# Performance work log

Measured on AMD Instinct MI355X. Metric: run time of the kernel, lower is better.

The kernel has to match this reference:

```python
import jax, jax.numpy as jnp
import numpy as np

N_GEN = 6
DIM = 1 << N_GEN  # 64
B, F = 256, 128
EPS = 1e-6


def _build_algebra():
    # Blades as bitmasks over N_GEN generators, canonical grade-then-lex order.
    blades = sorted(range(DIM), key=lambda b: (bin(b).count("1"), b))
    index = {b: i for i, b in enumerate(blades)}
    grades = np.array([bin(b).count("1") for b in blades], dtype=np.int64)
    cls = (grades % 4).astype(np.int32)  # quaternion-type class of each blade

    def swap_sign(a, b):
        s = 0
        a >>= 1
        while a:
            s += bin(a & b).count("1")
            a >>= 1
        return -1.0 if (s & 1) else 1.0

    # cayley[i, j, k] = coefficient of e_j in e_i * e_k (Euclidean metric, +1 squares)
    cayley = np.zeros((DIM, DIM, DIM), dtype=np.float32)
    for bi in range(DIM):
        for bk in range(DIM):
            cayley[index[bi], index[bi ^ bk], index[bk]] = swap_sign(bi, bk)

    # qt_geometric_product_paths: which (class_i, class_j, class_k) triples are nonzero
    paths = np.zeros((4, 4, 4), dtype=bool)
    i_, j_, k_ = np.nonzero(cayley)
    paths[cls[i_], cls[j_], cls[k_]] = True
    return cayley, cls, np.argwhere(paths).astype(np.int32)  # paths.sum() == 32


def setup_inputs() -> dict:
    cayley, cls, pidx = _build_algebra()
    P = pidx.shape[0]
    key = jax.random.key(0)
    k1, k2, k3 = jax.random.split(key, 3)
    x = jax.random.normal(k1, (B, F, DIM), jnp.float32)
    # reset_parameters: std = 1/sqrt(algebra.dim_generators + 1)
    w_gp = jax.random.normal(k2, (F, P), jnp.float32) / np.sqrt(N_GEN + 1)
    w_lin = jax.random.normal(k3, (F, F, 4), jnp.float32) / np.sqrt(F)
    b_lin = jnp.zeros((F,), jnp.float32)
    a_norm = jnp.zeros((F, 4), jnp.float32)  # normalization_init = 0
    return {"x": x, "w_gp": w_gp, "w_lin": w_lin, "b_lin": b_lin,
            "a_norm": a_norm, "cayley": jnp.asarray(cayley),
            "cls": jnp.asarray(cls), "path_idx": jnp.asarray(pidx)}


def reference(x, w_gp, w_lin, b_lin, a_norm, cayley, cls, path_idx):
    # --- QTLinear: per-QT-class channel mixing (weight shared within each class) ---
    w_lin_full = w_lin[:, :, cls]                          # [F_out, F_in, D]
    xr = jnp.einsum('bmi,nmi->bni', x, w_lin_full)         # [B, F, D]
    xr = xr.at[..., 0].add(b_lin)                          # bias on scalar blade only

    # --- QTNormalization: sigmoid-gated per-class norm, interpolated toward 1 ---
    sq = jnp.moveaxis(xr * xr, -1, 0)                      # [D, B, F]
    norms4 = jnp.sqrt(jax.ops.segment_sum(sq, cls, num_segments=4))  # [4, B, F]
    norms4 = jnp.moveaxis(norms4, 0, -1)                   # [B, F, 4]
    gated = jax.nn.sigmoid(a_norm) * (norms4 - 1.0) + 1.0  # [B, F, 4]
    xr = xr / (gated[..., cls] + EPS)                      # broadcast class norm to blades

    # --- _get_weight: scatter path weights into [F,4,4,4], expand to [F,D,D,D] ---
    # (scatter + repeat_interleave + permutation collapses to a class-index gather)
    F_ = w_gp.shape[0]
    full4 = jnp.zeros((F_, 4, 4, 4), x.dtype).at[
        :, path_idx[:, 0], path_idx[:, 1], path_idx[:, 2]].set(w_gp)
    w_full = full4[:, cls[:, None, None], cls[None, :, None], cls[None, None, :]]  # [F,D,D,D]
    weight = cayley[None] * w_full

    # --- weighted geometric product ---
    return jnp.einsum('bni,nijk,bnk->bnj', x, weight, xr)
```

## Files before the change

kernel.cpp:

```cpp
#include <hip/hip_runtime.h>
#include <hip/hip_bf16.h>

namespace alg {
constexpr int pc(int v) { int c = 0; while (v) { c += v & 1; v >>= 1; } return c; }
constexpr int swap_sign_i(int a, int b) {
  int s = 0; a >>= 1;
  while (a) { s += pc(a & b); a >>= 1; }
  return (s & 1) ? -1 : 1;
}
struct Tables {
  int blade[64]; int index[64]; int cls[64];
  int itab[64][64]; int sgn[64][64]; int ct[64][64];
  constexpr Tables() : blade{}, index{}, cls{}, itab{}, sgn{}, ct{} {
    int pos = 0;
    for (int g = 0; g <= 6; ++g)
      for (int b = 0; b < 64; ++b)
        if (pc(b) == g) { blade[pos] = b; index[b] = pos; ++pos; }
    for (int i = 0; i < 64; ++i) cls[i] = pc(blade[i]) & 3;
    for (int J = 0; J < 64; ++J)
      for (int K = 0; K < 64; ++K) {
        int bj = blade[J], bk = blade[K], bi = bj ^ bk;
        int I = index[bi];
        itab[J][K] = I;
        sgn[J][K] = swap_sign_i(bi, bk);
        ct[J][K] = cls[I] * 16 + cls[J] * 4 + cls[K];
      }
  }
};
constexpr Tables T{};
}

__device__ __forceinline__ float rfl(float v) {
  return __uint_as_float(__builtin_amdgcn_readfirstlane(__float_as_uint(v)));
}

__global__ __launch_bounds__(256) void kprep(
    const float* __restrict__ x, const float* __restrict__ wlin,
    const float* __restrict__ wgp, const int* __restrict__ pidx, int P,
    float* __restrict__ xT, float* __restrict__ Wt, float* __restrict__ g) {
  int bid = blockIdx.x;
  if (bid < 512) {
    __shared__ float tile[64 * 65];
    int m = bid >> 2, bc = (bid & 3) << 6;
    int lane = threadIdx.x & 63, row = threadIdx.x >> 6;
#pragma unroll
    for (int p = 0; p < 16; ++p) {
      int b = p * 4 + row;
      tile[lane * 65 + b] = x[(bc + b) * 8192 + m * 64 + lane];
    }
    __syncthreads();
#pragma unroll
    for (int p = 0; p < 16; ++p) {
      int il = p * 4 + row;
      xT[il * 32768 + m * 256 + bc + lane] = tile[il * 65 + lane];
    }
  } else if (bid < 768) {
    int id = (bid - 512) * 256 + threadIdx.x;
    int n = id & 127, m = (id >> 7) & 127, c = id >> 14;
    Wt[c * 16384 + m * 128 + n] = wlin[n * 512 + m * 4 + c];
  } else {
    int id = (bid - 768) * 256 + threadIdx.x;
    int n = id >> 6, t = id & 63;
    int ti = t >> 4, tj = (t >> 2) & 3, tk = t & 3;
    float v = 0.f;
    for (int p = 0; p < P; ++p)
      if (pidx[p * 3] == ti && pidx[p * 3 + 1] == tj && pidx[p * 3 + 2] == tk)
        v = wgp[n * P + p];
    g[n * 64 + t] = v;
  }
}

__global__ __launch_bounds__(256, 4) void klin(
    const float* __restrict__ xT, const float* __restrict__ Wt,
    const float* __restrict__ blin, float* __restrict__ xrT) {
  int wid = __builtin_amdgcn_readfirstlane(blockIdx.x * 4 + (threadIdx.x >> 6));
  int lane = threadIdx.x & 63;
  int i = wid & 63;
  int nt = (wid >> 6) & 7;
  int bc = (wid >> 9) << 6;
  int ci = alg::T.cls[i];

  const float* xp = xT + i * 32768 + bc + lane;
  const float* wp = Wt + ci * 16384 + nt * 16;
  float acc[16];
#pragma unroll
  for (int t = 0; t < 16; ++t) acc[t] = 0.f;

#pragma unroll 4
  for (int m = 0; m < 128; ++m) {
    float xv = xp[m * 256];
#pragma unroll
    for (int t = 0; t < 16; ++t) acc[t] = fmaf(xv, wp[m * 128 + t], acc[t]);
  }
  if (i == 0) {
#pragma unroll
    for (int t = 0; t < 16; ++t) acc[t] += blin[nt * 16 + t];
  }
#pragma unroll
  for (int t = 0; t < 16; ++t)
    xrT[(nt * 16 + t) * 16384 + i * 256 + bc + lane] = acc[t];
}

template <int JW>
__device__ __forceinline__ void prod_body(
    const float* __restrict__ xT, const float* __restrict__ xr,
    const float* __restrict__ g, const float* __restrict__ an,
    float* __restrict__ out, float* __restrict__ ot, int n, int bc, int lane) {
  float xv[64], rv[64];
#pragma unroll
  for (int i = 0; i < 64; ++i) xv[i] = xT[i * 32768 + n * 256 + bc + lane];
#pragma unroll
  for (int i = 0; i < 64; ++i) rv[i] = xr[n * 16384 + i * 256 + bc + lane];

  float gl[64];
#pragma unroll
  for (int t = 0; t < 64; ++t) gl[t] = rfl(g[n * 64 + t]);

  float s[4] = {0.f, 0.f, 0.f, 0.f};
#pragma unroll
  for (int i = 0; i < 64; ++i) {
    const int c = alg::T.cls[i];
    s[c] = fmaf(rv[i], rv[i], s[c]);
  }
  float r[4];
#pragma unroll
  for (int c = 0; c < 4; ++c) {
    float a = rfl(an[n * 4 + c]);
    float sig = 1.f / (1.f + __expf(-a));
    float gate = sig * (sqrtf(s[c]) - 1.f) + 1.f;
    r[c] = 1.f / (gate + 1e-6f);
  }
#pragma unroll
  for (int i = 0; i < 64; ++i) rv[i] *= r[alg::T.cls[i]];

  float acc[16];
#pragma unroll
  for (int jj = 0; jj < 16; ++jj) acc[jj] = 0.f;
#pragma unroll
  for (int k = 0; k < 64; ++k) {
#pragma unroll
    for (int jj = 0; jj < 16; ++jj) {
      const int j = JW * 16 + jj;
      const int ii = alg::T.itab[j][k];
      const int tt = alg::T.ct[j][k];
      float t = xv[ii] * rv[k];
      acc[jj] = fmaf(alg::T.sgn[j][k] > 0 ? gl[tt] : -gl[tt], t, acc[jj]);
    }
  }

#pragma unroll
  for (int jj = 0; jj < 16; ++jj) ot[jj * 68 + lane] = acc[jj];
  __builtin_amdgcn_s_waitcnt(0);
#pragma unroll
  for (int p = 0; p < 16; ++p) {
    int j = lane & 15, br = p * 4 + (lane >> 4);
    out[(bc + br) * 8192 + n * 64 + JW * 16 + j] = ot[j * 68 + br];
  }
}

__global__ __launch_bounds__(256, 2) void kprod(
    const float* __restrict__ xT, const float* __restrict__ xr,
    const float* __restrict__ g, const float* __restrict__ an,
    float* __restrict__ out) {
  __shared__ float ot[4][16 * 68];
  int bid = blockIdx.x;
  int n = bid >> 2;
  int bc = (bid & 3) << 6;
  int jw = threadIdx.x >> 6;
  int lane = threadIdx.x & 63;
  switch (jw) {
    case 0: prod_body<0>(xT, xr, g, an, out, ot[0], n, bc, lane); break;
    case 1: prod_body<1>(xT, xr, g, an, out, ot[1], n, bc, lane); break;
    case 2: prod_body<2>(xT, xr, g, an, out, ot[2], n, bc, lane); break;
    case 3: prod_body<3>(xT, xr, g, an, out, ot[3], n, bc, lane); break;
  }
}

extern "C" void kernel_launch(void* const* d_in, const int* in_sizes, int n_in,
                              void* d_out, int out_size, void* d_ws, size_t ws_size,
                              hipStream_t stream) {
  (void)n_in; (void)out_size; (void)ws_size;
  const float* x    = (const float*)d_in[0];
  const float* wgp  = (const float*)d_in[1];
  const float* wlin = (const float*)d_in[2];
  const float* blin = (const float*)d_in[3];
  const float* an   = (const float*)d_in[4];
  const int*   pidx = (const int*)d_in[7];
  int P = in_sizes[7] / 3;

  float* ws  = (float*)d_ws;
  float* xT  = ws;
  float* xrT = ws + 2097152;
  float* Wt  = ws + 4194304;
  float* g   = ws + 4259840;

  kprep<<<800, 256, 0, stream>>>(x, wlin, wgp, pidx, P, xT, Wt, g);
  klin<<<512, 256, 0, stream>>>(xT, Wt, blin, xrT);
  kprod<<<512, 256, 0, stream>>>(xT, xrT, g, an, (float*)d_out);
}
```

Before: 111.7 us.

## Stage x and xr tiles in shared memory for klin and kprod

klin now runs 512-thread blocks that each stage the 128x64 x slice for one blade and batch chunk in LDS once. All 8 output-feature waves then share that slice, and the weights are read as float4. kprod loads the x and xr tiles cooperatively into LDS once per block instead of having each of its 4 waves re-read all 64 blades from global memory. This cuts redundant global traffic, at the cost of extra barriers, more LDS use and fewer blocks in klin.

```diff
diff --git a/kernel.cpp b/kernel.cpp
--- a/kernel.cpp
+++ b/kernel.cpp
@@ -70,69 +70,59 @@
   }
 }
 
-__global__ __launch_bounds__(256, 4) void klin(
+__global__ __launch_bounds__(512) void klin(
     const float* __restrict__ xT, const float* __restrict__ Wt,
     const float* __restrict__ blin, float* __restrict__ xrT) {
-  int wid = __builtin_amdgcn_readfirstlane(blockIdx.x * 4 + (threadIdx.x >> 6));
-  int lane = threadIdx.x & 63;
-  int i = wid & 63;
-  int nt = (wid >> 6) & 7;
-  int bc = (wid >> 9) << 6;
+  __shared__ float xs[128 * 64];
+  int bid = blockIdx.x;
+  int i = bid >> 2;
+  int bc = (bid & 3) << 6;
   int ci = alg::T.cls[i];
-
-  const float* xp = xT + i * 32768 + bc + lane;
-  const float* wp = Wt + ci * 16384 + nt * 16;
+  int t = threadIdx.x;
+  {
+    int b = t & 63, m0 = t >> 6;
+    const float* src = xT + i * 32768 + bc + b;
+#pragma unroll
+    for (int r = 0; r < 16; ++r) {
+      int m = m0 * 16 + r;
+      xs[m * 64 + b] = src[m * 256];
+    }
+  }
+  __syncthreads();
+
+  int w = t >> 6;
+  int lane = t & 63;
+  const float4* wp4 = (const float4*)Wt + ci * 4096 + w * 4;
   float acc[16];
 #pragma unroll
-  for (int t = 0; t < 16; ++t) acc[t] = 0.f;
+  for (int q = 0; q < 16; ++q) acc[q] = 0.f;
 
 #pragma unroll 4
   for (int m = 0; m < 128; ++m) {
-    float xv = xp[m * 256];
-#pragma unroll
-    for (int t = 0; t < 16; ++t) acc[t] = fmaf(xv, wp[m * 128 + t], acc[t]);
+    float xv = xs[m * 64 + lane];
+#pragma unroll
+    for (int q = 0; q < 4; ++q) {
+      float4 wv = wp4[m * 32 + q];
+      acc[q * 4 + 0] = fmaf(xv, wv.x, acc[q * 4 + 0]);
+      acc[q * 4 + 1] = fmaf(xv, wv.y, acc[q * 4 + 1]);
+      acc[q * 4 + 2] = fmaf(xv, wv.z, acc[q * 4 + 2]);
+      acc[q * 4 + 3] = fmaf(xv, wv.w, acc[q * 4 + 3]);
+    }
   }
   if (i == 0) {
 #pragma unroll
-    for (int t = 0; t < 16; ++t) acc[t] += blin[nt * 16 + t];
-  }
-#pragma unroll
-  for (int t = 0; t < 16; ++t)
-    xrT[(nt * 16 + t) * 16384 + i * 256 + bc + lane] = acc[t];
+    for (int q = 0; q < 16; ++q) acc[q] += blin[w * 16 + q];
+  }
+#pragma unroll
+  for (int q = 0; q < 16; ++q)
+    xrT[(w * 16 + q) * 16384 + i * 256 + bc + lane] = acc[q];
 }
 
 template <int JW>
 __device__ __forceinline__ void prod_body(
-    const float* __restrict__ xT, const float* __restrict__ xr,
-    const float* __restrict__ g, const float* __restrict__ an,
-    float* __restrict__ out, float* __restrict__ ot, int n, int bc, int lane) {
-  float xv[64], rv[64];
-#pragma unroll
-  for (int i = 0; i < 64; ++i) xv[i] = xT[i * 32768 + n * 256 + bc + lane];
-#pragma unroll
-  for (int i = 0; i < 64; ++i) rv[i] = xr[n * 16384 + i * 256 + bc + lane];
-
-  float gl[64];
-#pragma unroll
-  for (int t = 0; t < 64; ++t) gl[t] = rfl(g[n * 64 + t]);
-
-  float s[4] = {0.f, 0.f, 0.f, 0.f};
-#pragma unroll
-  for (int i = 0; i < 64; ++i) {
-    const int c = alg::T.cls[i];
-    s[c] = fmaf(rv[i], rv[i], s[c]);
-  }
-  float r[4];
-#pragma unroll
-  for (int c = 0; c < 4; ++c) {
-    float a = rfl(an[n * 4 + c]);
-    float sig = 1.f / (1.f + __expf(-a));
-    float gate = sig * (sqrtf(s[c]) - 1.f) + 1.f;
-    r[c] = 1.f / (gate + 1e-6f);
-  }
-#pragma unroll
-  for (int i = 0; i < 64; ++i) rv[i] *= r[alg::T.cls[i]];
-
+    const float* __restrict__ xv, const float* __restrict__ rv,
+    const float* __restrict__ gl, float* __restrict__ out,
+    float* __restrict__ ot, int n, int bc, int lane) {
   float acc[16];
 #pragma unroll
   for (int jj = 0; jj < 16; ++jj) acc[jj] = 0.f;
@@ -147,7 +137,6 @@
       acc[jj] = fmaf(alg::T.sgn[j][k] > 0 ? gl[tt] : -gl[tt], t, acc[jj]);
     }
   }
-
 #pragma unroll
   for (int jj = 0; jj < 16; ++jj) ot[jj * 68 + lane] = acc[jj];
   __builtin_amdgcn_s_waitcnt(0);
@@ -162,17 +151,64 @@
     const float* __restrict__ xT, const float* __restrict__ xr,
     const float* __restrict__ g, const float* __restrict__ an,
     float* __restrict__ out) {
-  __shared__ float ot[4][16 * 68];
+  __shared__ float smem[8192];
+  float* xs = smem;
+  float* rs = smem + 4096;
   int bid = blockIdx.x;
   int n = bid >> 2;
   int bc = (bid & 3) << 6;
-  int jw = threadIdx.x >> 6;
-  int lane = threadIdx.x & 63;
-  switch (jw) {
-    case 0: prod_body<0>(xT, xr, g, an, out, ot[0], n, bc, lane); break;
-    case 1: prod_body<1>(xT, xr, g, an, out, ot[1], n, bc, lane); break;
-    case 2: prod_body<2>(xT, xr, g, an, out, ot[2], n, bc, lane); break;
-    case 3: prod_body<3>(xT, xr, g, an, out, ot[3], n, bc, lane); break;
+  int t = threadIdx.x;
+  int w = t >> 6;
+  int lane = t & 63;
+
+  {
+    int b = t & 63, i0 = t >> 6;
+    const float* sx = xT + n * 256 + bc + b;
+    const float* sr = xr + n * 16384 + bc + b;
+#pragma unroll
+    for (int r = 0; r < 16; ++r) {
+      int i = i0 * 16 + r;
+      xs[i * 64 + b] = sx[i * 32768];
+      rs[i * 64 + b] = sr[i * 256];
+    }
+  }
+  __syncthreads();
+
+  float xv[64], rv[64];
+#pragma unroll
+  for (int i = 0; i < 64; ++i) xv[i] = xs[i * 64 + lane];
+#pragma unroll
+  for (int i = 0; i < 64; ++i) rv[i] = rs[i * 64 + lane];
+
+  float gl[64];
+#pragma unroll
+  for (int q = 0; q < 64; ++q) gl[q] = rfl(g[n * 64 + q]);
+
+  float s[4] = {0.f, 0.f, 0.f, 0.f};
+#pragma unroll
+  for (int i = 0; i < 64; ++i) {
+    const int c = alg::T.cls[i];
+    s[c] = fmaf(rv[i], rv[i], s[c]);
+  }
+  float r[4];
+#pragma unroll
+  for (int c = 0; c < 4; ++c) {
+    float a = rfl(an[n * 4 + c]);
+    float sig = 1.f / (1.f + __expf(-a));
+    float gate = sig * (sqrtf(s[c]) - 1.f) + 1.f;
+    r[c] = 1.f / (gate + 1e-6f);
+  }
+#pragma unroll
+  for (int i = 0; i < 64; ++i) rv[i] *= r[alg::T.cls[i]];
+
+  __syncthreads();
+  float* ot = smem + w * 1088;
+
+  switch (w) {
+    case 0: prod_body<0>(xv, rv, gl, out, ot, n, bc, lane); break;
+    case 1: prod_body<1>(xv, rv, gl, out, ot, n, bc, lane); break;
+    case 2: prod_body<2>(xv, rv, gl, out, ot, n, bc, lane); break;
+    case 3: prod_body<3>(xv, rv, gl, out, ot, n, bc, lane); break;
   }
 }
 
@@ -195,6 +231,6 @@
   float* g   = ws + 4259840;
 
   kprep<<<800, 256, 0, stream>>>(x, wlin, wgp, pidx, P, xT, Wt, g);
-  klin<<<512, 256, 0, stream>>>(xT, Wt, blin, xrT);
+  klin<<<256, 512, 0, stream>>>(xT, Wt, blin, xrT);
   kprod<<<512, 256, 0, stream>>>(xT, xrT, g, an, (float*)d_out);
 }
```

Result: slower. 129.2 us (+15.7%).
